# Kernel tuning notes

Hardware: AMD Instinct MI355X
Metric: run time of the kernel (lower is better)

## Reference

```python
import jax, jax.numpy as jnp
import numpy as np

NUM_USERS = 150000
NUM_ITEMS = 80000
N_NODES = NUM_USERS + NUM_ITEMS
NNZ = 5000000
LATENT_DIM = 64
N_LAYERS = 3


def setup_inputs() -> dict:
    key = jax.random.key(0)
    k1, k2, k3, k4, k5 = jax.random.split(key, 5)
    user_emb = 0.1 * jax.random.normal(k1, (NUM_USERS, LATENT_DIM), dtype=jnp.float32)
    item_emb = 0.1 * jax.random.normal(k2, (NUM_ITEMS, LATENT_DIM), dtype=jnp.float32)
    adj_rows = jax.random.randint(k3, (NNZ,), 0, N_NODES, dtype=jnp.int32)
    adj_cols = jax.random.randint(k4, (NNZ,), 0, N_NODES, dtype=jnp.int32)
    # scale values ~ 1/avg_degree so propagation is stable (mimics sym-normalized adjacency)
    adj_vals = jax.random.uniform(k5, (NNZ,), dtype=jnp.float32) * (N_NODES / NNZ)
    return {"user_emb": user_emb, "item_emb": item_emb,
            "adj_rows": adj_rows, "adj_cols": adj_cols, "adj_vals": adj_vals}


def _spmm(rows, cols, vals, x):
    # y[r] = sum_{e: rows[e]==r} vals[e] * x[cols[e]]  == torch.sparse.mm(G, x)
    return jax.ops.segment_sum(vals[:, None] * x[cols], rows, num_segments=N_NODES)


def reference(user_emb, item_emb, adj_rows, adj_cols, adj_vals):
    all_emb = jnp.concatenate([user_emb, item_emb], axis=0)  # [N, d]
    acc = all_emb
    for _ in range(N_LAYERS):
        all_emb = _spmm(adj_rows, adj_cols, adj_vals, all_emb)
        acc = acc + all_emb
    light_out = acc / (N_LAYERS + 1)  # mean over stacked layer embeddings
    users = light_out[:NUM_USERS]
    items = light_out[NUM_USERS:]
    return users, items
```

## Files before the change

kernel.cpp:

```cpp
#include <hip/hip_runtime.h>

#define NUM_USERS 150000
#define NUM_ITEMS 80000
#define N_NODES   230000
#define NNZ       5000000
#define DIM       64

#define SB_SHIFT 10
#define SB_SIZE  1024
#define NUM_SB   ((N_NODES + SB_SIZE - 1) / SB_SIZE)
#define SB_CAP   32768
#define PA_ITEMS 4

#define VAL_MAX   0.046f
#define VAL_ENC   (16384.0f / VAL_MAX)
#define VAL_SCALE (VAL_MAX / 16384.0f)

__device__ __forceinline__ float bf2f(unsigned short h) {
    return __uint_as_float(((unsigned int)h) << 16);
}
__device__ __forceinline__ unsigned short f2bf(float f) {
    unsigned int u = __float_as_uint(f);
    u += 0x7FFFu + ((u >> 16) & 1u);
    return (unsigned short)(u >> 16);
}
__device__ __forceinline__ float bflo(unsigned int u) {
    return __uint_as_float(u << 16);
}
__device__ __forceinline__ float bfhi(unsigned int u) {
    return __uint_as_float(u & 0xFFFF0000u);
}
__device__ __forceinline__ unsigned int pk2(float a, float b) {
    return (unsigned int)f2bf(a) | ((unsigned int)f2bf(b) << 16);
}

__global__ void init_kernel(const float* __restrict__ u,
                            const float* __restrict__ it,
                            unsigned short* __restrict__ x) {
    long i = (long)blockIdx.x * blockDim.x + threadIdx.x;
    const long n4  = (long)N_NODES * DIM / 4;
    const long iu4 = (long)NUM_USERS * DIM / 4;
    if (i >= n4) return;
    float4 v = (i < iu4) ? ((const float4*)u)[i]
                         : ((const float4*)it)[i - iu4];
    ushort4 h;
    h.x = f2bf(v.x); h.y = f2bf(v.y); h.z = f2bf(v.z); h.w = f2bf(v.w);
    ((ushort4*)x)[i] = h;
}

__global__ void cursor_init_kernel(int* __restrict__ bucket_cursor) {
    int t = threadIdx.x;
    if (t < NUM_SB) bucket_cursor[t] = t * SB_CAP;
}

__global__ void partA_kernel(const int* __restrict__ rows,
                             const int* __restrict__ cols,
                             const float* __restrict__ vals,
                             int* __restrict__ bucket_cursor,
                             unsigned int* __restrict__ Xe,
                             unsigned short* __restrict__ Xr) {
    __shared__ int bcnt[NUM_SB];
    __shared__ int bbase[NUM_SB];
    const int t = threadIdx.x;
    const long tile = 1024L * PA_ITEMS;
    for (long base = (long)blockIdx.x * tile; base < NNZ;
         base += (long)gridDim.x * tile) {
        for (int j = t; j < NUM_SB; j += 1024) bcnt[j] = 0;
        __syncthreads();
        int b[PA_ITEMS], rank[PA_ITEMS], rl[PA_ITEMS];
        unsigned int pk[PA_ITEMS];
        bool ok[PA_ITEMS];
        for (int k = 0; k < PA_ITEMS; ++k) {
            long e = base + (long)k * 1024 + t;
            ok[k] = (e < NNZ);
            if (ok[k]) {
                int r = rows[e];
                b[k]  = r >> SB_SHIFT;
                rl[k] = r & (SB_SIZE - 1);
                int vc = (int)(vals[e] * VAL_ENC + 0.5f);
                vc = min(vc, 16383);
                pk[k] = ((unsigned int)vc << 18) | (unsigned int)cols[e];
                rank[k] = atomicAdd(&bcnt[b[k]], 1);
            }
        }
        __syncthreads();
        for (int j = t; j < NUM_SB; j += 1024)
            if (bcnt[j] > 0) bbase[j] = atomicAdd(&bucket_cursor[j], bcnt[j]);
        __syncthreads();
        for (int k = 0; k < PA_ITEMS; ++k)
            if (ok[k]) {
                int pos = bbase[b[k]] + rank[k];
                Xe[pos] = pk[k];
                Xr[pos] = (unsigned short)rl[k];
            }
        __syncthreads();
    }
}

__global__ void sb_scan_kernel(const int* __restrict__ bucket_cursor,
                               int* __restrict__ sb_base) {
    __shared__ int lds[256];
    const int t = threadIdx.x;
    const int s = (t < NUM_SB) ? (bucket_cursor[t] - t * SB_CAP) : 0;
    lds[t] = s;
    __syncthreads();
    for (int off = 1; off < 256; off <<= 1) {
        int add = (t >= off) ? lds[t - off] : 0;
        __syncthreads();
        lds[t] += add;
        __syncthreads();
    }
    if (t < NUM_SB) sb_base[t] = lds[t] - s;
    if (t == 0) sb_base[NUM_SB] = NNZ;
}

__global__ void partB_kernel(const unsigned int* __restrict__ Xe,
                             const unsigned short* __restrict__ Xr,
                             const int* __restrict__ sb_base,
                             int* __restrict__ row_start,
                             unsigned int* __restrict__ edges) {
    __shared__ int hist[SB_SIZE];
    __shared__ int scan[SB_SIZE];
    const int b    = blockIdx.x;
    const int t    = threadIdx.x;
    const int rlo  = b << SB_SHIFT;
    const int nrows = min(SB_SIZE, N_NODES - rlo);
    const int xoff = b * SB_CAP;
    const int base = sb_base[b];
    const int cnt  = sb_base[b + 1] - base;
    hist[t] = 0;
    __syncthreads();
    for (int i = t; i < cnt; i += 1024)
        atomicAdd(&hist[Xr[xoff + i]], 1);
    __syncthreads();
    const int v = hist[t];
    scan[t] = v;
    __syncthreads();
    for (int off = 1; off < 1024; off <<= 1) {
        int add = (t >= off) ? scan[t - off] : 0;
        __syncthreads();
        scan[t] += add;
        __syncthreads();
    }
    const int rs = base + (scan[t] - v);
    if (t < nrows) row_start[rlo + t] = rs;
    hist[t] = rs;
    __syncthreads();
    for (int i = t; i < cnt; i += 1024) {
        int rl = Xr[xoff + i];
        int pos = atomicAdd(&hist[rl], 1);
        edges[pos] = Xe[xoff + i];
    }
    if (b == 0 && t == 0) row_start[N_NODES] = NNZ;
}

#define FMA8(v, h) \
    a0 = fmaf((v), bflo((h).x), a0); a1 = fmaf((v), bfhi((h).x), a1); \
    a2 = fmaf((v), bflo((h).y), a2); a3 = fmaf((v), bfhi((h).y), a3); \
    a4 = fmaf((v), bflo((h).z), a4); a5 = fmaf((v), bfhi((h).z), a5); \
    a6 = fmaf((v), bflo((h).w), a6); a7 = fmaf((v), bfhi((h).w), a7);

__global__ void spmm_kernel(const int* __restrict__ row_start,
                            const unsigned int* __restrict__ edges,
                            const unsigned short* __restrict__ x,
                            unsigned short* __restrict__ y) {
    const int lane = threadIdx.x & 63;
    const int oct  = lane >> 3;
    const int fo   = (lane & 7) << 3;
    int row = (int)((blockIdx.x * blockDim.x + threadIdx.x) >> 6);
    if (row >= N_NODES) return;
    row = __builtin_amdgcn_readfirstlane(row);
    const int s = row_start[row];
    const int e = row_start[row + 1];
    const unsigned short* xf = x + fo;
    float a0 = 0, a1 = 0, a2 = 0, a3 = 0, a4 = 0, a5 = 0, a6 = 0, a7 = 0;
    int i = s;
    for (; i + 16 <= e; i += 16) {
        unsigned int ea = edges[i + oct];
        unsigned int eb = edges[i + 8 + oct];
        const uint4 ha = *(const uint4*)(xf + (((long)(ea & 0x3FFFF)) << 6));
        const uint4 hb = *(const uint4*)(xf + (((long)(eb & 0x3FFFF)) << 6));
        const float va = (float)(ea >> 18) * VAL_SCALE;
        const float vb = (float)(eb >> 18) * VAL_SCALE;
        FMA8(va, ha);
        FMA8(vb, hb);
    }
    if (i + 8 <= e) {
        unsigned int ec = edges[i + oct];
        const uint4 h = *(const uint4*)(xf + (((long)(ec & 0x3FFFF)) << 6));
        const float v = (float)(ec >> 18) * VAL_SCALE;
        FMA8(v, h);
        i += 8;
    }
    if (i + oct < e) {
        unsigned int ec = edges[i + oct];
        const uint4 h = *(const uint4*)(xf + (((long)(ec & 0x3FFFF)) << 6));
        const float v = (float)(ec >> 18) * VAL_SCALE;
        FMA8(v, h);
    }
    a0 += __shfl_xor(a0, 8);  a1 += __shfl_xor(a1, 8);
    a2 += __shfl_xor(a2, 8);  a3 += __shfl_xor(a3, 8);
    a4 += __shfl_xor(a4, 8);  a5 += __shfl_xor(a5, 8);
    a6 += __shfl_xor(a6, 8);  a7 += __shfl_xor(a7, 8);
    a0 += __shfl_xor(a0, 16); a1 += __shfl_xor(a1, 16);
    a2 += __shfl_xor(a2, 16); a3 += __shfl_xor(a3, 16);
    a4 += __shfl_xor(a4, 16); a5 += __shfl_xor(a5, 16);
    a6 += __shfl_xor(a6, 16); a7 += __shfl_xor(a7, 16);
    a0 += __shfl_xor(a0, 32); a1 += __shfl_xor(a1, 32);
    a2 += __shfl_xor(a2, 32); a3 += __shfl_xor(a3, 32);
    a4 += __shfl_xor(a4, 32); a5 += __shfl_xor(a5, 32);
    a6 += __shfl_xor(a6, 32); a7 += __shfl_xor(a7, 32);
    if (oct == 0) {
        uint4 w;
        w.x = pk2(a0, a1); w.y = pk2(a2, a3);
        w.z = pk2(a4, a5); w.w = pk2(a6, a7);
        *(uint4*)(y + (((long)row) << 6) + fo) = w;
    }
}

__global__ void spmm_final_kernel(const int* __restrict__ row_start,
                                  const unsigned int* __restrict__ edges,
                                  const unsigned short* __restrict__ y2,
                                  const unsigned short* __restrict__ y1,
                                  const float* __restrict__ u,
                                  const float* __restrict__ it,
                                  float* __restrict__ acc) {
    const int lane = threadIdx.x & 63;
    const int oct  = lane >> 3;
    const int fo   = (lane & 7) << 3;
    int row = (int)((blockIdx.x * blockDim.x + threadIdx.x) >> 6);
    if (row >= N_NODES) return;
    row = __builtin_amdgcn_readfirstlane(row);
    const int s = row_start[row];
    const int e = row_start[row + 1];
    const unsigned short* xf = y2 + fo;
    float a0 = 0, a1 = 0, a2 = 0, a3 = 0, a4 = 0, a5 = 0, a6 = 0, a7 = 0;
    int i = s;
    for (; i + 16 <= e; i += 16) {
        unsigned int ea = edges[i + oct];
        unsigned int eb = edges[i + 8 + oct];
        const uint4 ha = *(const uint4*)(xf + (((long)(ea & 0x3FFFF)) << 6));
        const uint4 hb = *(const uint4*)(xf + (((long)(eb & 0x3FFFF)) << 6));
        const float va = (float)(ea >> 18) * VAL_SCALE;
        const float vb = (float)(eb >> 18) * VAL_SCALE;
        FMA8(va, ha);
        FMA8(vb, hb);
    }
    if (i + 8 <= e) {
        unsigned int ec = edges[i + oct];
        const uint4 h = *(const uint4*)(xf + (((long)(ec & 0x3FFFF)) << 6));
        const float v = (float)(ec >> 18) * VAL_SCALE;
        FMA8(v, h);
        i += 8;
    }
    if (i + oct < e) {
        unsigned int ec = edges[i + oct];
        const uint4 h = *(const uint4*)(xf + (((long)(ec & 0x3FFFF)) << 6));
        const float v = (float)(ec >> 18) * VAL_SCALE;
        FMA8(v, h);
    }
    a0 += __shfl_xor(a0, 8);  a1 += __shfl_xor(a1, 8);
    a2 += __shfl_xor(a2, 8);  a3 += __shfl_xor(a3, 8);
    a4 += __shfl_xor(a4, 8);  a5 += __shfl_xor(a5, 8);
    a6 += __shfl_xor(a6, 8);  a7 += __shfl_xor(a7, 8);
    a0 += __shfl_xor(a0, 16); a1 += __shfl_xor(a1, 16);
    a2 += __shfl_xor(a2, 16); a3 += __shfl_xor(a3, 16);
    a4 += __shfl_xor(a4, 16); a5 += __shfl_xor(a5, 16);
    a6 += __shfl_xor(a6, 16); a7 += __shfl_xor(a7, 16);
    a0 += __shfl_xor(a0, 32); a1 += __shfl_xor(a1, 32);
    a2 += __shfl_xor(a2, 32); a3 += __shfl_xor(a3, 32);
    a4 += __shfl_xor(a4, 32); a5 += __shfl_xor(a5, 32);
    a6 += __shfl_xor(a6, 32); a7 += __shfl_xor(a7, 32);
    if (oct == 0) {
        const long o = (((long)row) << 6) + fo;
        const float* x0p = (row < NUM_USERS) ? (u + o)
                         : (it + o - (((long)NUM_USERS) << 6));
        const float4 xa = *(const float4*)(x0p);
        const float4 xb = *(const float4*)(x0p + 4);
        const uint4 h1 = *(const uint4*)(y1 + o);
        const uint4 h2 = *(const uint4*)(y2 + o);
        float4 ra, rb;
        ra.x = (xa.x + bflo(h1.x) + bflo(h2.x) + a0) * 0.25f;
        ra.y = (xa.y + bfhi(h1.x) + bfhi(h2.x) + a1) * 0.25f;
        ra.z = (xa.z + bflo(h1.y) + bflo(h2.y) + a2) * 0.25f;
        ra.w = (xa.w + bfhi(h1.y) + bfhi(h2.y) + a3) * 0.25f;
        rb.x = (xb.x + bflo(h1.z) + bflo(h2.z) + a4) * 0.25f;
        rb.y = (xb.y + bfhi(h1.z) + bfhi(h2.z) + a5) * 0.25f;
        rb.z = (xb.z + bflo(h1.w) + bflo(h2.w) + a6) * 0.25f;
        rb.w = (xb.w + bfhi(h1.w) + bfhi(h2.w) + a7) * 0.25f;
        *(float4*)(acc + o) = ra;
        *(float4*)(acc + o + 4) = rb;
    }
}

extern "C" void kernel_launch(void* const* d_in, const int* in_sizes, int n_in,
                              void* d_out, int out_size, void* d_ws, size_t ws_size,
                              hipStream_t stream) {
    const float* u    = (const float*)d_in[0];
    const float* it   = (const float*)d_in[1];
    const int*   rows = (const int*)d_in[2];
    const int*   cols = (const int*)d_in[3];
    const float* vals = (const float*)d_in[4];
    float* acc = (float*)d_out;

    const size_t bufBf = (size_t)N_NODES * DIM * 2;
    const size_t edgeB = (size_t)NNZ * 4;
    const size_t XeB   = (size_t)NUM_SB * SB_CAP * 4;
    const size_t XrB   = (size_t)NUM_SB * SB_CAP * 2;
    const size_t nodeB = 921600;
    char* ws = (char*)d_ws;
    unsigned short* buf0 = (unsigned short*)(ws);
    unsigned short* buf1 = (unsigned short*)(ws + bufBf);
    unsigned short* buf2 = (unsigned short*)(ws + 2 * bufBf);
    unsigned int*   edges = (unsigned int*)(ws + 3 * bufBf);
    unsigned int*   Xe   = (unsigned int*)(ws + 3 * bufBf + edgeB);
    unsigned short* Xr   = (unsigned short*)(ws + 3 * bufBf + edgeB + XeB);
    char* p              = ws + 3 * bufBf + edgeB + XeB + XrB;
    int* row_start       = (int*)(p);   p += nodeB;
    int* bucket_cursor   = (int*)(p);   p += 1024;
    int* sb_base         = (int*)(p);

    const int n4 = N_NODES * DIM / 4;
    const int ewGrid = (n4 + 255) / 256;

    init_kernel<<<ewGrid, 256, 0, stream>>>(u, it, buf0);

    cursor_init_kernel<<<1, 256, 0, stream>>>(bucket_cursor);
    partA_kernel<<<512, 1024, 0, stream>>>(rows, cols, vals, bucket_cursor, Xe, Xr);
    sb_scan_kernel<<<1, 256, 0, stream>>>(bucket_cursor, sb_base);
    partB_kernel<<<NUM_SB, 1024, 0, stream>>>(Xe, Xr, sb_base, row_start, edges);

    const int spmmGrid = (N_NODES * 64 + 255) / 256;
    spmm_kernel<<<spmmGrid, 256, 0, stream>>>(row_start, edges, buf0, buf1);
    spmm_kernel<<<spmmGrid, 256, 0, stream>>>(row_start, edges, buf1, buf2);
    spmm_final_kernel<<<spmmGrid, 256, 0, stream>>>(row_start, edges, buf2,
                                                    buf1, u, it, acc);
}
```

Before: 563.5 us.

## Bucket rows by degree and assign eight rows per wavefront in SpMM

Adds three kernels that histogram row degrees, scan the counts and scatter row descriptors (row, start, degree) sorted by degree, reusing the Xe buffer to hold them. The SpMM kernels now map eight degree-similar rows to each wavefront, one per 8-lane group, and loop to the group's maximum degree. This drops the cross-lane shuffle reduction and the per-row wave underutilisation of the old one-row-per-wave scheme. In exchange there is extra preprocessing, uncoalesced edge index loads per lane, and padded iterations for the rows in a group whose degree is below the group maximum.

```diff
diff --git a/kernel.cpp b/kernel.cpp
--- a/kernel.cpp
+++ b/kernel.cpp
@@ -11,6 +11,8 @@
 #define NUM_SB   ((N_NODES + SB_SIZE - 1) / SB_SIZE)
 #define SB_CAP   32768
 #define PA_ITEMS 4
+
+#define DBINS 256
 
 #define VAL_MAX   0.046f
 #define VAL_ENC   (16384.0f / VAL_MAX)
@@ -48,9 +50,11 @@
     ((ushort4*)x)[i] = h;
 }
 
-__global__ void cursor_init_kernel(int* __restrict__ bucket_cursor) {
+__global__ void cursor_init_kernel(int* __restrict__ bucket_cursor,
+                                   int* __restrict__ dhist) {
     int t = threadIdx.x;
     if (t < NUM_SB) bucket_cursor[t] = t * SB_CAP;
+    dhist[t] = 0;
 }
 
 __global__ void partA_kernel(const int* __restrict__ rows,
@@ -154,126 +158,150 @@
     if (b == 0 && t == 0) row_start[N_NODES] = NNZ;
 }
 
+__global__ void deg_hist_kernel(const int* __restrict__ row_start,
+                                int* __restrict__ dhist) {
+    __shared__ int h[DBINS];
+    const int t = threadIdx.x;
+    h[t] = 0;
+    __syncthreads();
+    int r = blockIdx.x * 256 + t;
+    if (r < N_NODES) {
+        int d = row_start[r + 1] - row_start[r];
+        atomicAdd(&h[min(d, DBINS - 1)], 1);
+    }
+    __syncthreads();
+    if (h[t]) atomicAdd(&dhist[t], h[t]);
+}
+
+__global__ void deg_scan_kernel(const int* __restrict__ dhist,
+                                int* __restrict__ dcur) {
+    __shared__ int lds[DBINS];
+    const int t = threadIdx.x;
+    const int s = dhist[t];
+    lds[t] = s;
+    __syncthreads();
+    for (int off = 1; off < DBINS; off <<= 1) {
+        int add = (t >= off) ? lds[t - off] : 0;
+        __syncthreads();
+        lds[t] += add;
+        __syncthreads();
+    }
+    dcur[t] = lds[t] - s;
+}
+
+__global__ void deg_scatter_kernel(const int* __restrict__ row_start,
+                                   int* __restrict__ dcur,
+                                   uint4* __restrict__ desc) {
+    __shared__ int bcnt[DBINS];
+    __shared__ int bbase[DBINS];
+    const int t = threadIdx.x;
+    bcnt[t] = 0;
+    __syncthreads();
+    int r = blockIdx.x * 256 + t;
+    int bin = 0, rank = 0, s = 0, d = 0;
+    const bool ok = (r < N_NODES);
+    if (ok) {
+        s = row_start[r];
+        d = row_start[r + 1] - s;
+        bin = min(d, DBINS - 1);
+        rank = atomicAdd(&bcnt[bin], 1);
+    }
+    __syncthreads();
+    if (bcnt[t]) bbase[t] = atomicAdd(&dcur[t], bcnt[t]);
+    __syncthreads();
+    if (ok)
+        desc[bbase[bin] + rank] =
+            make_uint4((unsigned)r, (unsigned)s, (unsigned)d, 0u);
+}
+
 #define FMA8(v, h) \
     a0 = fmaf((v), bflo((h).x), a0); a1 = fmaf((v), bfhi((h).x), a1); \
     a2 = fmaf((v), bflo((h).y), a2); a3 = fmaf((v), bfhi((h).y), a3); \
     a4 = fmaf((v), bflo((h).z), a4); a5 = fmaf((v), bfhi((h).z), a5); \
     a6 = fmaf((v), bflo((h).w), a6); a7 = fmaf((v), bfhi((h).w), a7);
 
-__global__ void spmm_kernel(const int* __restrict__ row_start,
-                            const unsigned int* __restrict__ edges,
-                            const unsigned short* __restrict__ x,
-                            unsigned short* __restrict__ y) {
+__global__ __launch_bounds__(256)
+void spmm8_kernel(const uint4* __restrict__ desc,
+                  const unsigned int* __restrict__ edges,
+                  const unsigned short* __restrict__ x,
+                  unsigned short* __restrict__ y) {
     const int lane = threadIdx.x & 63;
     const int oct  = lane >> 3;
     const int fo   = (lane & 7) << 3;
-    int row = (int)((blockIdx.x * blockDim.x + threadIdx.x) >> 6);
-    if (row >= N_NODES) return;
-    row = __builtin_amdgcn_readfirstlane(row);
-    const int s = row_start[row];
-    const int e = row_start[row + 1];
+    const long wv  = (long)blockIdx.x * 4 + (threadIdx.x >> 6);
+    const long rowIdx = wv * 8 + oct;
+    const bool valid = (rowIdx < N_NODES);
+    const uint4 dsc = desc[valid ? rowIdx : (N_NODES - 1)];
+    const int r = (int)dsc.x;
+    const int s = (int)dsc.y;
+    const int deg = valid ? (int)dsc.z : 0;
+    int dm = deg;
+    dm = max(dm, __shfl_xor(dm, 8));
+    dm = max(dm, __shfl_xor(dm, 16));
+    dm = max(dm, __shfl_xor(dm, 32));
+    dm = __builtin_amdgcn_readfirstlane(dm);
     const unsigned short* xf = x + fo;
     float a0 = 0, a1 = 0, a2 = 0, a3 = 0, a4 = 0, a5 = 0, a6 = 0, a7 = 0;
-    int i = s;
-    for (; i + 16 <= e; i += 16) {
-        unsigned int ea = edges[i + oct];
-        unsigned int eb = edges[i + 8 + oct];
-        const uint4 ha = *(const uint4*)(xf + (((long)(ea & 0x3FFFF)) << 6));
-        const uint4 hb = *(const uint4*)(xf + (((long)(eb & 0x3FFFF)) << 6));
-        const float va = (float)(ea >> 18) * VAL_SCALE;
-        const float vb = (float)(eb >> 18) * VAL_SCALE;
-        FMA8(va, ha);
-        FMA8(vb, hb);
-    }
-    if (i + 8 <= e) {
-        unsigned int ec = edges[i + oct];
-        const uint4 h = *(const uint4*)(xf + (((long)(ec & 0x3FFFF)) << 6));
-        const float v = (float)(ec >> 18) * VAL_SCALE;
-        FMA8(v, h);
-        i += 8;
-    }
-    if (i + oct < e) {
-        unsigned int ec = edges[i + oct];
-        const uint4 h = *(const uint4*)(xf + (((long)(ec & 0x3FFFF)) << 6));
-        const float v = (float)(ec >> 18) * VAL_SCALE;
-        FMA8(v, h);
-    }
-    a0 += __shfl_xor(a0, 8);  a1 += __shfl_xor(a1, 8);
-    a2 += __shfl_xor(a2, 8);  a3 += __shfl_xor(a3, 8);
-    a4 += __shfl_xor(a4, 8);  a5 += __shfl_xor(a5, 8);
-    a6 += __shfl_xor(a6, 8);  a7 += __shfl_xor(a7, 8);
-    a0 += __shfl_xor(a0, 16); a1 += __shfl_xor(a1, 16);
-    a2 += __shfl_xor(a2, 16); a3 += __shfl_xor(a3, 16);
-    a4 += __shfl_xor(a4, 16); a5 += __shfl_xor(a5, 16);
-    a6 += __shfl_xor(a6, 16); a7 += __shfl_xor(a7, 16);
-    a0 += __shfl_xor(a0, 32); a1 += __shfl_xor(a1, 32);
-    a2 += __shfl_xor(a2, 32); a3 += __shfl_xor(a3, 32);
-    a4 += __shfl_xor(a4, 32); a5 += __shfl_xor(a5, 32);
-    a6 += __shfl_xor(a6, 32); a7 += __shfl_xor(a7, 32);
-    if (oct == 0) {
+    for (int i = 0; i < dm; i += 2) {
+        const int o0 = (i     < deg) ? (s + i)     : 0;
+        const int o1 = (i + 1 < deg) ? (s + i + 1) : 0;
+        const unsigned int e0 = edges[o0];
+        const unsigned int e1 = edges[o1];
+        const uint4 ha = *(const uint4*)(xf + (((long)(e0 & 0x3FFFF)) << 6));
+        const uint4 hb = *(const uint4*)(xf + (((long)(e1 & 0x3FFFF)) << 6));
+        const float v0 = (i     < deg) ? (float)(e0 >> 18) * VAL_SCALE : 0.0f;
+        const float v1 = (i + 1 < deg) ? (float)(e1 >> 18) * VAL_SCALE : 0.0f;
+        FMA8(v0, ha);
+        FMA8(v1, hb);
+    }
+    if (valid) {
         uint4 w;
         w.x = pk2(a0, a1); w.y = pk2(a2, a3);
         w.z = pk2(a4, a5); w.w = pk2(a6, a7);
-        *(uint4*)(y + (((long)row) << 6) + fo) = w;
-    }
-}
-
-__global__ void spmm_final_kernel(const int* __restrict__ row_start,
-                                  const unsigned int* __restrict__ edges,
-                                  const unsigned short* __restrict__ y2,
-                                  const unsigned short* __restrict__ y1,
-                                  const float* __restrict__ u,
-                                  const float* __restrict__ it,
-                                  float* __restrict__ acc) {
+        *(uint4*)(y + (((long)r) << 6) + fo) = w;
+    }
+}
+
+__global__ __launch_bounds__(256)
+void spmm_final8_kernel(const uint4* __restrict__ desc,
+                        const unsigned int* __restrict__ edges,
+                        const unsigned short* __restrict__ y2,
+                        const unsigned short* __restrict__ y1,
+                        const float* __restrict__ u,
+                        const float* __restrict__ it,
+                        float* __restrict__ acc) {
     const int lane = threadIdx.x & 63;
     const int oct  = lane >> 3;
     const int fo   = (lane & 7) << 3;
-    int row = (int)((blockIdx.x * blockDim.x + threadIdx.x) >> 6);
-    if (row >= N_NODES) return;
-    row = __builtin_amdgcn_readfirstlane(row);
-    const int s = row_start[row];
-    const int e = row_start[row + 1];
+    const long wv  = (long)blockIdx.x * 4 + (threadIdx.x >> 6);
+    const long rowIdx = wv * 8 + oct;
+    const bool valid = (rowIdx < N_NODES);
+    const uint4 dsc = desc[valid ? rowIdx : (N_NODES - 1)];
+    const int r = (int)dsc.x;
+    const int s = (int)dsc.y;
+    const int deg = valid ? (int)dsc.z : 0;
+    int dm = deg;
+    dm = max(dm, __shfl_xor(dm, 8));
+    dm = max(dm, __shfl_xor(dm, 16));
+    dm = max(dm, __shfl_xor(dm, 32));
+    dm = __builtin_amdgcn_readfirstlane(dm);
     const unsigned short* xf = y2 + fo;
     float a0 = 0, a1 = 0, a2 = 0, a3 = 0, a4 = 0, a5 = 0, a6 = 0, a7 = 0;
-    int i = s;
-    for (; i + 16 <= e; i += 16) {
-        unsigned int ea = edges[i + oct];
-        unsigned int eb = edges[i + 8 + oct];
-        const uint4 ha = *(const uint4*)(xf + (((long)(ea & 0x3FFFF)) << 6));
-        const uint4 hb = *(const uint4*)(xf + (((long)(eb & 0x3FFFF)) << 6));
-        const float va = (float)(ea >> 18) * VAL_SCALE;
-        const float vb = (float)(eb >> 18) * VAL_SCALE;
-        FMA8(va, ha);
-        FMA8(vb, hb);
-    }
-    if (i + 8 <= e) {
-        unsigned int ec = edges[i + oct];
-        const uint4 h = *(const uint4*)(xf + (((long)(ec & 0x3FFFF)) << 6));
-        const float v = (float)(ec >> 18) * VAL_SCALE;
-        FMA8(v, h);
-        i += 8;
-    }
-    if (i + oct < e) {
-        unsigned int ec = edges[i + oct];
-        const uint4 h = *(const uint4*)(xf + (((long)(ec & 0x3FFFF)) << 6));
-        const float v = (float)(ec >> 18) * VAL_SCALE;
-        FMA8(v, h);
-    }
-    a0 += __shfl_xor(a0, 8);  a1 += __shfl_xor(a1, 8);
-    a2 += __shfl_xor(a2, 8);  a3 += __shfl_xor(a3, 8);
-    a4 += __shfl_xor(a4, 8);  a5 += __shfl_xor(a5, 8);
-    a6 += __shfl_xor(a6, 8);  a7 += __shfl_xor(a7, 8);
-    a0 += __shfl_xor(a0, 16); a1 += __shfl_xor(a1, 16);
-    a2 += __shfl_xor(a2, 16); a3 += __shfl_xor(a3, 16);
-    a4 += __shfl_xor(a4, 16); a5 += __shfl_xor(a5, 16);
-    a6 += __shfl_xor(a6, 16); a7 += __shfl_xor(a7, 16);
-    a0 += __shfl_xor(a0, 32); a1 += __shfl_xor(a1, 32);
-    a2 += __shfl_xor(a2, 32); a3 += __shfl_xor(a3, 32);
-    a4 += __shfl_xor(a4, 32); a5 += __shfl_xor(a5, 32);
-    a6 += __shfl_xor(a6, 32); a7 += __shfl_xor(a7, 32);
-    if (oct == 0) {
-        const long o = (((long)row) << 6) + fo;
-        const float* x0p = (row < NUM_USERS) ? (u + o)
+    for (int i = 0; i < dm; i += 2) {
+        const int o0 = (i     < deg) ? (s + i)     : 0;
+        const int o1 = (i + 1 < deg) ? (s + i + 1) : 0;
+        const unsigned int e0 = edges[o0];
+        const unsigned int e1 = edges[o1];
+        const uint4 ha = *(const uint4*)(xf + (((long)(e0 & 0x3FFFF)) << 6));
+        const uint4 hb = *(const uint4*)(xf + (((long)(e1 & 0x3FFFF)) << 6));
+        const float v0 = (i     < deg) ? (float)(e0 >> 18) * VAL_SCALE : 0.0f;
+        const float v1 = (i + 1 < deg) ? (float)(e1 >> 18) * VAL_SCALE : 0.0f;
+        FMA8(v0, ha);
+        FMA8(v1, hb);
+    }
+    if (valid) {
+        const long o = (((long)r) << 6) + fo;
+        const float* x0p = (r < NUM_USERS) ? (u + o)
                          : (it + o - (((long)NUM_USERS) << 6));
         const float4 xa = *(const float4*)(x0p);
         const float4 xb = *(const float4*)(x0p + 4);
@@ -318,21 +346,30 @@
     char* p              = ws + 3 * bufBf + edgeB + XeB + XrB;
     int* row_start       = (int*)(p);   p += nodeB;
     int* bucket_cursor   = (int*)(p);   p += 1024;
-    int* sb_base         = (int*)(p);
+    int* sb_base         = (int*)(p);   p += 1024;
+    int* dhist           = (int*)(p);   p += DBINS * 4;
+    int* dcur            = (int*)(p);
+    uint4* desc          = (uint4*)Xe;
 
     const int n4 = N_NODES * DIM / 4;
     const int ewGrid = (n4 + 255) / 256;
+    const int rowBlocks = (N_NODES + 255) / 256;
 
     init_kernel<<<ewGrid, 256, 0, stream>>>(u, it, buf0);
 
-    cursor_init_kernel<<<1, 256, 0, stream>>>(bucket_cursor);
+    cursor_init_kernel<<<1, 256, 0, stream>>>(bucket_cursor, dhist);
     partA_kernel<<<512, 1024, 0, stream>>>(rows, cols, vals, bucket_cursor, Xe, Xr);
     sb_scan_kernel<<<1, 256, 0, stream>>>(bucket_cursor, sb_base);
     partB_kernel<<<NUM_SB, 1024, 0, stream>>>(Xe, Xr, sb_base, row_start, edges);
 
-    const int spmmGrid = (N_NODES * 64 + 255) / 256;
-    spmm_kernel<<<spmmGrid, 256, 0, stream>>>(row_start, edges, buf0, buf1);
-    spmm_kernel<<<spmmGrid, 256, 0, stream>>>(row_start, edges, buf1, buf2);
-    spmm_final_kernel<<<spmmGrid, 256, 0, stream>>>(row_start, edges, buf2,
-                                                    buf1, u, it, acc);
-}
+    deg_hist_kernel<<<rowBlocks, 256, 0, stream>>>(row_start, dhist);
+    deg_scan_kernel<<<1, DBINS, 0, stream>>>(dhist, dcur);
+    deg_scatter_kernel<<<rowBlocks, 256, 0, stream>>>(row_start, dcur, desc);
+
+    const long waves = (N_NODES + 7) / 8;
+    const int spmmGrid = (int)((waves + 3) / 4);
+    spmm8_kernel<<<spmmGrid, 256, 0, stream>>>(desc, edges, buf0, buf1);
+    spmm8_kernel<<<spmmGrid, 256, 0, stream>>>(desc, edges, buf1, buf2);
+    spmm_final8_kernel<<<spmmGrid, 256, 0, stream>>>(desc, edges, buf2,
+                                                     buf1, u, it, acc);
+}
```

New measurement: 604.0 us. +7.2%, slower.

## Process eight rows per wavefront in SpMM with 8-deep gather batching

Applied to the files above, without the earlier changes.

Changes the SpMM mapping from one row per 64-lane wavefront (edges split across lane octets, then a shuffle reduction) to eight rows per wavefront, one row per 8-lane group. Each group loops up to the wavefront's maximum degree, issuing eight edge loads and eight 16-byte feature gathers at a time before the FMAs. This removes the cross-lane reductions and the idle lanes on short-degree tails, and raises memory-level parallelism. In exchange, lanes whose row has a lower degree sit masked until the longest row in the wavefront finishes, and they still issue dummy loads of edge 0. Register pressure also rises from the eight buffered uint4 gathers.

```diff
diff --git a/kernel.cpp b/kernel.cpp
--- a/kernel.cpp
+++ b/kernel.cpp
@@ -12,13 +12,12 @@
 #define SB_CAP   32768
 #define PA_ITEMS 4
 
+#define NSLICES   (N_NODES / 8)
+
 #define VAL_MAX   0.046f
 #define VAL_ENC   (16384.0f / VAL_MAX)
 #define VAL_SCALE (VAL_MAX / 16384.0f)
 
-__device__ __forceinline__ float bf2f(unsigned short h) {
-    return __uint_as_float(((unsigned int)h) << 16);
-}
 __device__ __forceinline__ unsigned short f2bf(float f) {
     unsigned int u = __float_as_uint(f);
     u += 0x7FFFu + ((u >> 16) & 1u);
@@ -160,137 +159,109 @@
     a4 = fmaf((v), bflo((h).z), a4); a5 = fmaf((v), bfhi((h).z), a5); \
     a6 = fmaf((v), bflo((h).w), a6); a7 = fmaf((v), bfhi((h).w), a7);
 
-__global__ void spmm_kernel(const int* __restrict__ row_start,
-                            const unsigned int* __restrict__ edges,
-                            const unsigned short* __restrict__ x,
-                            unsigned short* __restrict__ y) {
+__global__ __launch_bounds__(256)
+void spmm8_kernel(const int* __restrict__ row_start,
+                  const unsigned int* __restrict__ edges,
+                  const unsigned short* __restrict__ x,
+                  unsigned short* __restrict__ y) {
     const int lane = threadIdx.x & 63;
     const int oct  = lane >> 3;
     const int fo   = (lane & 7) << 3;
-    int row = (int)((blockIdx.x * blockDim.x + threadIdx.x) >> 6);
-    if (row >= N_NODES) return;
-    row = __builtin_amdgcn_readfirstlane(row);
-    const int s = row_start[row];
-    const int e = row_start[row + 1];
+    const int wv   = blockIdx.x * 4 + (threadIdx.x >> 6);
+    if (wv >= NSLICES) return;
+    const int row = wv * 8 + oct;
+    const int s   = row_start[row];
+    const int deg = row_start[row + 1] - s;
+    int dm = deg;
+    dm = max(dm, __shfl_xor(dm, 8));
+    dm = max(dm, __shfl_xor(dm, 16));
+    dm = max(dm, __shfl_xor(dm, 32));
+    dm = __builtin_amdgcn_readfirstlane(dm);
     const unsigned short* xf = x + fo;
     float a0 = 0, a1 = 0, a2 = 0, a3 = 0, a4 = 0, a5 = 0, a6 = 0, a7 = 0;
-    int i = s;
-    for (; i + 16 <= e; i += 16) {
-        unsigned int ea = edges[i + oct];
-        unsigned int eb = edges[i + 8 + oct];
-        const uint4 ha = *(const uint4*)(xf + (((long)(ea & 0x3FFFF)) << 6));
-        const uint4 hb = *(const uint4*)(xf + (((long)(eb & 0x3FFFF)) << 6));
-        const float va = (float)(ea >> 18) * VAL_SCALE;
-        const float vb = (float)(eb >> 18) * VAL_SCALE;
-        FMA8(va, ha);
-        FMA8(vb, hb);
-    }
-    if (i + 8 <= e) {
-        unsigned int ec = edges[i + oct];
-        const uint4 h = *(const uint4*)(xf + (((long)(ec & 0x3FFFF)) << 6));
-        const float v = (float)(ec >> 18) * VAL_SCALE;
-        FMA8(v, h);
-        i += 8;
-    }
-    if (i + oct < e) {
-        unsigned int ec = edges[i + oct];
-        const uint4 h = *(const uint4*)(xf + (((long)(ec & 0x3FFFF)) << 6));
-        const float v = (float)(ec >> 18) * VAL_SCALE;
-        FMA8(v, h);
-    }
-    a0 += __shfl_xor(a0, 8);  a1 += __shfl_xor(a1, 8);
-    a2 += __shfl_xor(a2, 8);  a3 += __shfl_xor(a3, 8);
-    a4 += __shfl_xor(a4, 8);  a5 += __shfl_xor(a5, 8);
-    a6 += __shfl_xor(a6, 8);  a7 += __shfl_xor(a7, 8);
-    a0 += __shfl_xor(a0, 16); a1 += __shfl_xor(a1, 16);
-    a2 += __shfl_xor(a2, 16); a3 += __shfl_xor(a3, 16);
-    a4 += __shfl_xor(a4, 16); a5 += __shfl_xor(a5, 16);
-    a6 += __shfl_xor(a6, 16); a7 += __shfl_xor(a7, 16);
-    a0 += __shfl_xor(a0, 32); a1 += __shfl_xor(a1, 32);
-    a2 += __shfl_xor(a2, 32); a3 += __shfl_xor(a3, 32);
-    a4 += __shfl_xor(a4, 32); a5 += __shfl_xor(a5, 32);
-    a6 += __shfl_xor(a6, 32); a7 += __shfl_xor(a7, 32);
-    if (oct == 0) {
-        uint4 w;
-        w.x = pk2(a0, a1); w.y = pk2(a2, a3);
-        w.z = pk2(a4, a5); w.w = pk2(a6, a7);
-        *(uint4*)(y + (((long)row) << 6) + fo) = w;
-    }
-}
-
-__global__ void spmm_final_kernel(const int* __restrict__ row_start,
-                                  const unsigned int* __restrict__ edges,
-                                  const unsigned short* __restrict__ y2,
-                                  const unsigned short* __restrict__ y1,
-                                  const float* __restrict__ u,
-                                  const float* __restrict__ it,
-                                  float* __restrict__ acc) {
+    for (int i = 0; i < dm; i += 8) {
+        unsigned int ev[8];
+        uint4 h[8];
+        #pragma unroll
+        for (int k = 0; k < 8; ++k) {
+            const int o = (i + k < deg) ? (s + i + k) : 0;
+            ev[k] = edges[o];
+        }
+        #pragma unroll
+        for (int k = 0; k < 8; ++k)
+            h[k] = *(const uint4*)(xf + (((long)(ev[k] & 0x3FFFF)) << 6));
+        #pragma unroll
+        for (int k = 0; k < 8; ++k) {
+            const float v = (i + k < deg)
+                          ? (float)(ev[k] >> 18) * VAL_SCALE : 0.0f;
+            FMA8(v, h[k]);
+        }
+    }
+    uint4 w;
+    w.x = pk2(a0, a1); w.y = pk2(a2, a3);
+    w.z = pk2(a4, a5); w.w = pk2(a6, a7);
+    *(uint4*)(y + (((long)row) << 6) + fo) = w;
+}
+
+__global__ __launch_bounds__(256)
+void spmm_final8_kernel(const int* __restrict__ row_start,
+                        const unsigned int* __restrict__ edges,
+                        const unsigned short* __restrict__ y2,
+                        const unsigned short* __restrict__ y1,
+                        const float* __restrict__ u,
+                        const float* __restrict__ it,
+                        float* __restrict__ acc) {
     const int lane = threadIdx.x & 63;
     const int oct  = lane >> 3;
     const int fo   = (lane & 7) << 3;
-    int row = (int)((blockIdx.x * blockDim.x + threadIdx.x) >> 6);
-    if (row >= N_NODES) return;
-    row = __builtin_amdgcn_readfirstlane(row);
-    const int s = row_start[row];
-    const int e = row_start[row + 1];
+    const int wv   = blockIdx.x * 4 + (threadIdx.x >> 6);
+    if (wv >= NSLICES) return;
+    const int row = wv * 8 + oct;
+    const int s   = row_start[row];
+    const int deg = row_start[row + 1] - s;
+    int dm = deg;
+    dm = max(dm, __shfl_xor(dm, 8));
+    dm = max(dm, __shfl_xor(dm, 16));
+    dm = max(dm, __shfl_xor(dm, 32));
+    dm = __builtin_amdgcn_readfirstlane(dm);
     const unsigned short* xf = y2 + fo;
     float a0 = 0, a1 = 0, a2 = 0, a3 = 0, a4 = 0, a5 = 0, a6 = 0, a7 = 0;
-    int i = s;
-    for (; i + 16 <= e; i += 16) {
-        unsigned int ea = edges[i + oct];
-        unsigned int eb = edges[i + 8 + oct];
-        const uint4 ha = *(const uint4*)(xf + (((long)(ea & 0x3FFFF)) << 6));
-        const uint4 hb = *(const uint4*)(xf + (((long)(eb & 0x3FFFF)) << 6));
-        const float va = (float)(ea >> 18) * VAL_SCALE;
-        const float vb = (float)(eb >> 18) * VAL_SCALE;
-        FMA8(va, ha);
-        FMA8(vb, hb);
-    }
-    if (i + 8 <= e) {
-        unsigned int ec = edges[i + oct];
-        const uint4 h = *(const uint4*)(xf + (((long)(ec & 0x3FFFF)) << 6));
-        const float v = (float)(ec >> 18) * VAL_SCALE;
-        FMA8(v, h);
-        i += 8;
-    }
-    if (i + oct < e) {
-        unsigned int ec = edges[i + oct];
-        const uint4 h = *(const uint4*)(xf + (((long)(ec & 0x3FFFF)) << 6));
-        const float v = (float)(ec >> 18) * VAL_SCALE;
-        FMA8(v, h);
-    }
-    a0 += __shfl_xor(a0, 8);  a1 += __shfl_xor(a1, 8);
-    a2 += __shfl_xor(a2, 8);  a3 += __shfl_xor(a3, 8);
-    a4 += __shfl_xor(a4, 8);  a5 += __shfl_xor(a5, 8);
-    a6 += __shfl_xor(a6, 8);  a7 += __shfl_xor(a7, 8);
-    a0 += __shfl_xor(a0, 16); a1 += __shfl_xor(a1, 16);
-    a2 += __shfl_xor(a2, 16); a3 += __shfl_xor(a3, 16);
-    a4 += __shfl_xor(a4, 16); a5 += __shfl_xor(a5, 16);
-    a6 += __shfl_xor(a6, 16); a7 += __shfl_xor(a7, 16);
-    a0 += __shfl_xor(a0, 32); a1 += __shfl_xor(a1, 32);
-    a2 += __shfl_xor(a2, 32); a3 += __shfl_xor(a3, 32);
-    a4 += __shfl_xor(a4, 32); a5 += __shfl_xor(a5, 32);
-    a6 += __shfl_xor(a6, 32); a7 += __shfl_xor(a7, 32);
-    if (oct == 0) {
-        const long o = (((long)row) << 6) + fo;
-        const float* x0p = (row < NUM_USERS) ? (u + o)
-                         : (it + o - (((long)NUM_USERS) << 6));
-        const float4 xa = *(const float4*)(x0p);
-        const float4 xb = *(const float4*)(x0p + 4);
-        const uint4 h1 = *(const uint4*)(y1 + o);
-        const uint4 h2 = *(const uint4*)(y2 + o);
-        float4 ra, rb;
-        ra.x = (xa.x + bflo(h1.x) + bflo(h2.x) + a0) * 0.25f;
-        ra.y = (xa.y + bfhi(h1.x) + bfhi(h2.x) + a1) * 0.25f;
-        ra.z = (xa.z + bflo(h1.y) + bflo(h2.y) + a2) * 0.25f;
-        ra.w = (xa.w + bfhi(h1.y) + bfhi(h2.y) + a3) * 0.25f;
-        rb.x = (xb.x + bflo(h1.z) + bflo(h2.z) + a4) * 0.25f;
-        rb.y = (xb.y + bfhi(h1.z) + bfhi(h2.z) + a5) * 0.25f;
-        rb.z = (xb.z + bflo(h1.w) + bflo(h2.w) + a6) * 0.25f;
-        rb.w = (xb.w + bfhi(h1.w) + bfhi(h2.w) + a7) * 0.25f;
-        *(float4*)(acc + o) = ra;
-        *(float4*)(acc + o + 4) = rb;
-    }
+    for (int i = 0; i < dm; i += 8) {
+        unsigned int ev[8];
+        uint4 h[8];
+        #pragma unroll
+        for (int k = 0; k < 8; ++k) {
+            const int o = (i + k < deg) ? (s + i + k) : 0;
+            ev[k] = edges[o];
+        }
+        #pragma unroll
+        for (int k = 0; k < 8; ++k)
+            h[k] = *(const uint4*)(xf + (((long)(ev[k] & 0x3FFFF)) << 6));
+        #pragma unroll
+        for (int k = 0; k < 8; ++k) {
+            const float v = (i + k < deg)
+                          ? (float)(ev[k] >> 18) * VAL_SCALE : 0.0f;
+            FMA8(v, h[k]);
+        }
+    }
+    const long o = (((long)row) << 6) + fo;
+    const float* x0p = (row < NUM_USERS) ? (u + o)
+                     : (it + o - (((long)NUM_USERS) << 6));
+    const float4 xa = *(const float4*)(x0p);
+    const float4 xb = *(const float4*)(x0p + 4);
+    const uint4 h1 = *(const uint4*)(y1 + o);
+    const uint4 h2 = *(const uint4*)(y2 + o);
+    float4 ra, rb;
+    ra.x = (xa.x + bflo(h1.x) + bflo(h2.x) + a0) * 0.25f;
+    ra.y = (xa.y + bfhi(h1.x) + bfhi(h2.x) + a1) * 0.25f;
+    ra.z = (xa.z + bflo(h1.y) + bflo(h2.y) + a2) * 0.25f;
+    ra.w = (xa.w + bfhi(h1.y) + bfhi(h2.y) + a3) * 0.25f;
+    rb.x = (xb.x + bflo(h1.z) + bflo(h2.z) + a4) * 0.25f;
+    rb.y = (xb.y + bfhi(h1.z) + bfhi(h2.z) + a5) * 0.25f;
+    rb.z = (xb.z + bflo(h1.w) + bflo(h2.w) + a6) * 0.25f;
+    rb.w = (xb.w + bfhi(h1.w) + bfhi(h2.w) + a7) * 0.25f;
+    *(float4*)(acc + o) = ra;
+    *(float4*)(acc + o + 4) = rb;
 }
 
 extern "C" void kernel_launch(void* const* d_in, const int* in_sizes, int n_in,
@@ -330,9 +301,9 @@
     sb_scan_kernel<<<1, 256, 0, stream>>>(bucket_cursor, sb_base);
     partB_kernel<<<NUM_SB, 1024, 0, stream>>>(Xe, Xr, sb_base, row_start, edges);
 
-    const int spmmGrid = (N_NODES * 64 + 255) / 256;
-    spmm_kernel<<<spmmGrid, 256, 0, stream>>>(row_start, edges, buf0, buf1);
-    spmm_kernel<<<spmmGrid, 256, 0, stream>>>(row_start, edges, buf1, buf2);
-    spmm_final_kernel<<<spmmGrid, 256, 0, stream>>>(row_start, edges, buf2,
-                                                    buf1, u, it, acc);
-}
+    const int spmmGrid = (NSLICES + 3) / 4;
+    spmm8_kernel<<<spmmGrid, 256, 0, stream>>>(row_start, edges, buf0, buf1);
+    spmm8_kernel<<<spmmGrid, 256, 0, stream>>>(row_start, edges, buf1, buf2);
+    spmm_final8_kernel<<<spmmGrid, 256, 0, stream>>>(row_start, edges, buf2,
+                                                     buf1, u, it, acc);
+}
```

New measurement: 548.7 us. 2.6% less time.
